# Kernel optimization log

Hardware: AMD Instinct MI355X
Metric: run time of the kernel (lower is better)

Reference implementation:

```python
import jax, jax.numpy as jnp
import numpy as np

B, T, N, F_IN = 32, 64, 128, 16
H, SOUT = 64, 16
D = N * SOUT            # transformer d_model = 2048
NHEADS, DH = 16, 128
DFF, LAYERS = 2048, 2
NCLASSES, OUT = 8, 10
THR = 0.004             # edge threshold on sigmoid(V)/N


def setup_inputs():
    key = jax.random.key(0)
    ks = iter(jax.random.split(key, 40))
    r = lambda *s: jax.random.normal(next(ks), s, jnp.float32) * 0.02
    return {
        'X': jax.random.normal(next(ks), (B, T, N * F_IN), jnp.float32),
        'V_Adap': jax.random.normal(next(ks), (NCLASSES, N, N), jnp.float32),
        'Wl': r(F_IN, H), 'bl': jnp.zeros((H,)),
        'Wr': r(F_IN, H), 'br': jnp.zeros((H,)),
        'att': jax.random.normal(next(ks), (H,), jnp.float32) * 0.1,
        'gat_bias': jnp.zeros((H,)),
        'Wfc': r(H, SOUT), 'bfc': jnp.zeros((SOUT,)),
        'Wq': r(LAYERS, D, D), 'bq': jnp.zeros((LAYERS, D)),
        'Wk': r(LAYERS, D, D), 'bk': jnp.zeros((LAYERS, D)),
        'Wv': r(LAYERS, D, D), 'bv': jnp.zeros((LAYERS, D)),
        'Wo': r(LAYERS, D, D), 'bo': jnp.zeros((LAYERS, D)),
        'ln1_g': jnp.ones((LAYERS, D)), 'ln1_b': jnp.zeros((LAYERS, D)),
        'W1': r(LAYERS, D, DFF), 'b1': jnp.zeros((LAYERS, DFF)),
        'W2': r(LAYERS, DFF, D), 'b2': jnp.zeros((LAYERS, D)),
        'ln2_g': jnp.ones((LAYERS, D)), 'ln2_b': jnp.zeros((LAYERS, D)),
        'Wout': r(D, OUT), 'bout': jnp.zeros((OUT,)),
        'class_idx': 2,
    }


def _ln(x, g, b):
    mu = jnp.mean(x, -1, keepdims=True)
    var = jnp.var(x, -1, keepdims=True)
    return (x - mu) / jnp.sqrt(var + 1e-5) * g + b


def reference(X, V_Adap, Wl, bl, Wr, br, att, gat_bias, Wfc, bfc,
              Wq, bq, Wk, bk, Wv, bv, Wo, bo, ln1_g, ln1_b,
              W1, b1, W2, b2, ln2_g, ln2_b, Wout, bout, class_idx):
    # dynamic adjacency: sigmoid + scale + threshold (data-dependent sparsity as a mask)
    A = jax.nn.sigmoid(V_Adap[class_idx]) / N
    mask = (A > THR) | jnp.eye(N, dtype=bool)   # GATv2Conv default add_self_loops

    def gat_step(x_t):                           # x_t: (B, N, F_IN)
        xl = x_t @ Wl + bl                       # source transform (B, N, H)
        xr = x_t @ Wr + br                       # target transform (B, N, H)
        s = jax.nn.leaky_relu(xl[:, :, None, :] + xr[:, None, :, :], 0.2)  # (B, src, dst, H)
        e = jnp.where(mask[None], jnp.einsum('bijh,h->bij', s, att), -1e9)
        alpha = jax.nn.softmax(e, axis=1)        # softmax over sources per target node
        out = jnp.einsum('bij,bih->bjh', alpha, xl) + gat_bias
        return out @ Wfc + bfc                   # (B, N, SOUT)

    Xr = X.reshape(B, T, N, F_IN).transpose(1, 0, 2, 3)   # (T, B, N, F)
    spatial = jax.lax.map(gat_step, Xr)                   # (T, B, N, SOUT)
    h = spatial.transpose(1, 0, 2, 3).reshape(B, T, D)

    # post-norm TransformerEncoder (torch defaults: relu, d_ff=2048, no dropout at eval)
    for l in range(LAYERS):
        q = (h @ Wq[l] + bq[l]).reshape(B, T, NHEADS, DH).transpose(0, 2, 1, 3)
        k = (h @ Wk[l] + bk[l]).reshape(B, T, NHEADS, DH).transpose(0, 2, 1, 3)
        v = (h @ Wv[l] + bv[l]).reshape(B, T, NHEADS, DH).transpose(0, 2, 1, 3)
        aw = jax.nn.softmax(jnp.einsum('bhqd,bhkd->bhqk', q, k) / np.float32(np.sqrt(DH)), axis=-1)
        ao = jnp.einsum('bhqk,bhkd->bhqd', aw, v).transpose(0, 2, 1, 3).reshape(B, T, D)
        h = _ln(h + ao @ Wo[l] + bo[l], ln1_g[l], ln1_b[l])
        ff = jax.nn.relu(h @ W1[l] + b1[l]) @ W2[l] + b2[l]
        h = _ln(h + ff, ln2_g[l], ln2_b[l])

    return h[:, -1, :] @ Wout + bout             # (B, OUT)
```

## Files before the change

kernel.cpp:

```cpp
#include <hip/hip_runtime.h>
#include <cstdint>
#include <cstddef>


typedef unsigned short u16;
typedef __bf16 bf16x8 __attribute__((ext_vector_type(8)));
typedef float f32x4 __attribute__((ext_vector_type(4)));
typedef unsigned int u32x4 __attribute__((ext_vector_type(4)));
typedef float f32x4v __attribute__((ext_vector_type(4)));
typedef unsigned short u16x4 __attribute__((ext_vector_type(4)));

__device__ __forceinline__ u16 f2b(float f) {
  union { float f; unsigned u; } x; x.f = f;
  unsigned r = x.u + 0x7fffu + ((x.u >> 16) & 1u);
  return (u16)(r >> 16);
}
__device__ __forceinline__ float b2f(u16 s) {
  union { unsigned u; float f; } x; x.u = ((unsigned)s) << 16;
  return x.f;
}
__device__ __forceinline__ float b2f_lo(unsigned q) {
  union { unsigned u; float f; } x; x.u = q << 16;
  return x.f;
}
__device__ __forceinline__ float b2f_hi(unsigned q) {
  union { unsigned u; float f; } x; x.u = q & 0xffff0000u;
  return x.f;
}

__device__ __forceinline__ void gload_lds16(const void* g, void* l) {
  __builtin_amdgcn_global_load_lds(
      (const __attribute__((address_space(1))) unsigned int*)g,
      (__attribute__((address_space(3))) unsigned int*)l, 16, 0, 0);
}

__global__ __launch_bounds__(1024) void gat_kernel(
    const float* __restrict__ X, const float* __restrict__ V_Adap,
    const int* __restrict__ class_idx,
    const float* __restrict__ Wl, const float* __restrict__ bl,
    const float* __restrict__ Wr, const float* __restrict__ br,
    const float* __restrict__ att, const float* __restrict__ gat_bias,
    const float* __restrict__ Wfc, const float* __restrict__ bfc,
    float* __restrict__ h_f32, u16* __restrict__ h_b16)
{
  const int bt = blockIdx.x;
  const int tid = threadIdx.x;

  __shared__ __align__(16) float xlT[64 * 132];
  __shared__ __align__(16) float xrT[64 * 132];
  __shared__ __align__(16) u16   xlTb[64 * 136];
  __shared__ __align__(16) u16   esbT[128 * 136];
  __shared__ __align__(16) u16   aggb[128 * 72];
  __shared__ __align__(16) float WlT[64 * 20];
  __shared__ __align__(16) float WrT[64 * 20];
  __shared__ __align__(16) float WfcT[16 * 66];
  __shared__ float atts[64], bls[64], brs[64], gbias[64], bfcs[16];
  __shared__ float cls[128], crs[128], inv_s[128];
  __shared__ float red[8 * 128];

  {
    const int h = tid >> 4, f = tid & 15;
    WlT[h * 20 + f] = Wl[f * 64 + h];
    WrT[h * 20 + f] = Wr[f * 64 + h];
    WfcT[f * 66 + h] = Wfc[h * 16 + f];
  }
  if (tid < 64) { atts[tid] = att[tid]; bls[tid] = bl[tid]; brs[tid] = br[tid]; gbias[tid] = gat_bias[tid]; }
  if (tid < 16) bfcs[tid] = bfc[tid];
  const int cidx = *class_idx;
  __syncthreads();

  {
    const int n = tid >> 3, hq = tid & 7;
    const float* xp = X + (size_t)bt * 2048 + n * 16;
    float xv[16];
    #pragma unroll
    for (int f4 = 0; f4 < 4; f4++) {
      f32x4v t4 = ((const f32x4v*)xp)[f4];
      xv[f4 * 4 + 0] = t4[0]; xv[f4 * 4 + 1] = t4[1];
      xv[f4 * 4 + 2] = t4[2]; xv[f4 * 4 + 3] = t4[3];
    }
    #pragma unroll
    for (int k = 0; k < 8; k++) {
      const int h = hq + 8 * k;
      float al = bls[h], ar = brs[h];
      #pragma unroll
      for (int f4 = 0; f4 < 4; f4++) {
        f32x4v wl = *(const f32x4v*)&WlT[h * 20 + f4 * 4];
        f32x4v wr = *(const f32x4v*)&WrT[h * 20 + f4 * 4];
        #pragma unroll
        for (int f = 0; f < 4; f++) {
          al = fmaf(xv[f4 * 4 + f], wl[f], al);
          ar = fmaf(xv[f4 * 4 + f], wr[f], ar);
        }
      }
      xlT[h * 132 + n] = al;
      xrT[h * 132 + n] = ar;
      xlTb[h * 136 + n] = f2b(al);
    }
  }
  __syncthreads();

  if (tid < 256) {
    const int n = tid & 127;
    const float* srcT = (tid < 128) ? xlT : xrT;
    float s = 0.f;
    for (int h = 0; h < 64; h++) s = fmaf(atts[h], srcT[h * 132 + n], s);
    if (tid < 128) cls[n] = s; else crs[n] = s;
  }
  __syncthreads();

  {
    const int i0 = (tid >> 5) * 4;
    const int j0 = (tid & 31) * 4;
    float acc[4][4] = {};
    #pragma unroll 2
    for (int h = 0; h < 64; h++) {
      const float ah = atts[h];
      f32x4v xa = *(const f32x4v*)&xlT[h * 132 + i0];
      f32x4v xb = *(const f32x4v*)&xrT[h * 132 + j0];
      #pragma unroll
      for (int a = 0; a < 4; a++)
        #pragma unroll
        for (int b = 0; b < 4; b++)
          acc[a][b] = fmaf(ah, __builtin_fabsf(xa[a] + xb[b]), acc[a][b]);
    }
    const float* Vc = V_Adap + (size_t)cidx * 16384;
    float vm[4][4];
    #pragma unroll
    for (int a = 0; a < 4; a++) {
      f32x4v vc = *(const f32x4v*)&Vc[(size_t)(i0 + a) * 128 + j0];
      #pragma unroll
      for (int b = 0; b < 4; b++) vm[a][b] = vc[b];
    }
    #pragma unroll
    for (int b = 0; b < 4; b++) {
      const int j = j0 + b;
      const float ej = 0.6f * crs[j];
      u16x4 pk;
      #pragma unroll
      for (int a = 0; a < 4; a++) {
        const int i = i0 + a;
        const float e = ej + 0.6f * cls[i] + 0.4f * acc[a][b];
        const bool m = (vm[a][b] > 0.04800922f) || (i == j);
        pk[a] = f2b(m ? e : -1e9f);
      }
      *(u16x4*)&esbT[j * 136 + i0] = pk;
    }
  }
  __syncthreads();

  {
    const int j = tid >> 3, c = tid & 7;
    u16* rp = &esbT[j * 136 + c * 16];
    float ps = 0.f;
    #pragma unroll
    for (int half = 0; half < 2; half++) {
      u32x4 q = *(u32x4*)(rp + half * 8);
      #pragma unroll
      for (int w2 = 0; w2 < 4; w2++) {
        const float p0 = __expf(b2f_lo(q[w2]));
        const float p1 = __expf(b2f_hi(q[w2]));
        ps += p0 + p1;
        q[w2] = (unsigned)f2b(p0) | ((unsigned)f2b(p1) << 16);
      }
      *(u32x4*)(rp + half * 8) = q;
    }
    red[c * 128 + j] = ps;
  }
  __syncthreads();
  if (tid < 128) {
    float s = 0.f;
    #pragma unroll
    for (int c = 0; c < 8; c++) s += red[c * 128 + tid];
    inv_s[tid] = 1.f / s;
  }
  __syncthreads();

  {
    const int w = tid >> 6, lane = tid & 63;
    const int lq = lane >> 4, lr = lane & 15;
    const int jt = w >> 1, ht0 = (w & 1) * 2;
    f32x4 acc2[2] = {};
    #pragma unroll
    for (int ks = 0; ks < 4; ks++) {
      const bf16x8 af = __builtin_bit_cast(bf16x8,
          *(const u32x4*)&esbT[(jt * 16 + lr) * 136 + ks * 32 + lq * 8]);
      #pragma unroll
      for (int t = 0; t < 2; t++) {
        const bf16x8 bfb = __builtin_bit_cast(bf16x8,
            *(const u32x4*)&xlTb[((ht0 + t) * 16 + lr) * 136 + ks * 32 + lq * 8]);
        acc2[t] = __builtin_amdgcn_mfma_f32_16x16x32_bf16(af, bfb, acc2[t], 0, 0, 0);
      }
    }
    #pragma unroll
    for (int t = 0; t < 2; t++) {
      const int h = (ht0 + t) * 16 + lr;
      const float gb = gbias[h];
      #pragma unroll
      for (int r = 0; r < 4; r++) {
        const int j = jt * 16 + lq * 4 + r;
        aggb[j * 72 + h] = f2b(acc2[t][r] * inv_s[j] + gb);
      }
    }
  }
  __syncthreads();

  {
    const int j = tid >> 3, s0 = (tid & 7) * 2;
    float o0 = bfcs[s0], o1 = bfcs[s0 + 1];
    #pragma unroll
    for (int h8 = 0; h8 < 8; h8++) {
      u32x4 q = *(const u32x4*)&aggb[j * 72 + h8 * 8];
      #pragma unroll
      for (int w2 = 0; w2 < 4; w2++) {
        const int h = h8 * 8 + w2 * 2;
        const float a0 = b2f_lo(q[w2]);
        const float a1 = b2f_hi(q[w2]);
        o0 = fmaf(a0, WfcT[s0 * 66 + h], o0);
        o1 = fmaf(a0, WfcT[(s0 + 1) * 66 + h], o1);
        o0 = fmaf(a1, WfcT[s0 * 66 + h + 1], o0);
        o1 = fmaf(a1, WfcT[(s0 + 1) * 66 + h + 1], o1);
      }
    }
    const size_t off = (size_t)bt * 2048 + j * 16 + s0;
    h_f32[off] = o0; h_f32[off + 1] = o1;
    h_b16[off] = f2b(o0); h_b16[off + 1] = f2b(o1);
  }
}

struct TransArgs {
  const float* s0; const float* s1; const float* s2;
  u16* d0; u16* d1; u16* d2;
};

__global__ __launch_bounds__(256) void transpose_cast(TransArgs p)
{
  const float* src = (blockIdx.z == 0) ? p.s0 : (blockIdx.z == 1) ? p.s1 : p.s2;
  u16* dst = (blockIdx.z == 0) ? p.d0 : (blockIdx.z == 1) ? p.d1 : p.d2;
  __shared__ u16 tile[64][66];
  const int k0 = blockIdx.y * 64, n0 = blockIdx.x * 64;
  const int tid = threadIdx.x;
  const int c = tid & 63, rb = tid >> 6;
  #pragma unroll
  for (int r = 0; r < 16; r++) {
    const int k = rb + r * 4;
    tile[k][c] = f2b(src[(size_t)(k0 + k) * 2048 + n0 + c]);
  }
  __syncthreads();
  #pragma unroll
  for (int r = 0; r < 16; r++) {
    const int n = rb + r * 4;
    dst[(size_t)(n0 + n) * 2048 + k0 + c] = tile[c][n];
  }
}

struct GemmArgs {
  const u16* A;
  const u16* Bt0; const u16* Bt1; const u16* Bt2;
  const float* b0; const float* b1; const float* b2;
  void* C0; void* C1; void* C2;
  int N; int K;
};

template <int MODE>
__global__ __launch_bounds__(256) void gemm_bt(GemmArgs g)
{
  const int z = blockIdx.z;
  const u16* Bt = (z == 0) ? g.Bt0 : (z == 1) ? g.Bt1 : g.Bt2;
  const float* bias = (z == 0) ? g.b0 : (z == 1) ? g.b1 : g.b2;
  void* C = (z == 0) ? g.C0 : (z == 1) ? g.C1 : g.C2;
  const int N = g.N, K = g.K;
  const int m0 = blockIdx.y * 128, n0 = blockIdx.x * 128;

  __shared__ __align__(16) u16 As[128 * 32];
  __shared__ __align__(16) u16 Bs[128 * 32];

  const int tid = threadIdx.x;
  const int lane = tid & 63, w = tid >> 6;
  const int srow = w * 16 + (lane >> 2);
  const int scol = (lane & 3) * 8;
  const u16* gA = g.A + (size_t)(m0 + srow) * K + scol;
  const u16* gB = Bt + (size_t)(n0 + srow) * K + scol;
  u16* lA0 = &As[(w * 16) * 32];
  u16* lA1 = &As[(64 + w * 16) * 32];
  u16* lB0 = &Bs[(w * 16) * 32];
  u16* lB1 = &Bs[(64 + w * 16) * 32];

  const int wm = (w >> 1) * 64, wn = (w & 1) * 64;
  const int lq = lane >> 4, lr = lane & 15;

  f32x4 acc[4][4] = {};

  for (int k0 = 0; k0 < K; k0 += 32) {
    gload_lds16(gA + k0, lA0);
    gload_lds16(gA + (size_t)64 * K + k0, lA1);
    gload_lds16(gB + k0, lB0);
    gload_lds16(gB + (size_t)64 * K + k0, lB1);
    __syncthreads();

    bf16x8 af[4], bf[4];
    #pragma unroll
    for (int i = 0; i < 4; i++) {
      af[i] = __builtin_bit_cast(bf16x8, *(const u32x4*)&As[(wm + i * 16 + lr) * 32 + lq * 8]);
      bf[i] = __builtin_bit_cast(bf16x8, *(const u32x4*)&Bs[(wn + i * 16 + lr) * 32 + lq * 8]);
    }
    #pragma unroll
    for (int mi = 0; mi < 4; mi++)
      #pragma unroll
      for (int ni = 0; ni < 4; ni++)
        acc[mi][ni] = __builtin_amdgcn_mfma_f32_16x16x32_bf16(af[mi], bf[ni], acc[mi][ni], 0, 0, 0);
    __syncthreads();
  }

  #pragma unroll
  for (int ni = 0; ni < 4; ni++) {
    const int col = n0 + wn + ni * 16 + lr;
    const float bv = bias[col];
    #pragma unroll
    for (int mi = 0; mi < 4; mi++) {
      #pragma unroll
      for (int r = 0; r < 4; r++) {
        const int row = m0 + wm + mi * 16 + lq * 4 + r;
        float v = acc[mi][ni][r] + bv;
        if (MODE == 0) {
          ((float*)C)[(size_t)row * N + col] = v;
        } else {
          if (MODE == 2) v = fmaxf(v, 0.f);
          ((u16*)C)[(size_t)row * N + col] = f2b(v);
        }
      }
    }
  }
}

template <int MODE>
__global__ __launch_bounds__(256) void gemm_bt64(GemmArgs g)
{
  const u16* Bt = g.Bt0;
  const float* bias = g.b0;
  void* C = g.C0;
  const int N = g.N, K = g.K;
  const int m0 = blockIdx.y * 128, n0 = blockIdx.x * 64;

  __shared__ __align__(16) u16 As[128 * 32];
  __shared__ __align__(16) u16 Bs[64 * 32];

  const int tid = threadIdx.x;
  const int lane = tid & 63, w = tid >> 6;
  const int srow = w * 16 + (lane >> 2);
  const int scol = (lane & 3) * 8;
  const u16* gA = g.A + (size_t)(m0 + srow) * K + scol;
  const u16* gB = Bt + (size_t)(n0 + srow) * K + scol;
  u16* lA0 = &As[(w * 16) * 32];
  u16* lA1 = &As[(64 + w * 16) * 32];
  u16* lB0 = &Bs[(w * 16) * 32];

  const int wm = w * 32;
  const int lq = lane >> 4, lr = lane & 15;

  f32x4 acc[2][4] = {};

  for (int k0 = 0; k0 < K; k0 += 32) {
    gload_lds16(gA + k0, lA0);
    gload_lds16(gA + (size_t)64 * K + k0, lA1);
    gload_lds16(gB + k0, lB0);
    __syncthreads();

    bf16x8 af[2], bf[4];
    #pragma unroll
    for (int i = 0; i < 2; i++)
      af[i] = __builtin_bit_cast(bf16x8, *(const u32x4*)&As[(wm + i * 16 + lr) * 32 + lq * 8]);
    #pragma unroll
    for (int i = 0; i < 4; i++)
      bf[i] = __builtin_bit_cast(bf16x8, *(const u32x4*)&Bs[(i * 16 + lr) * 32 + lq * 8]);
    #pragma unroll
    for (int mi = 0; mi < 2; mi++)
      #pragma unroll
      for (int ni = 0; ni < 4; ni++)
        acc[mi][ni] = __builtin_amdgcn_mfma_f32_16x16x32_bf16(af[mi], bf[ni], acc[mi][ni], 0, 0, 0);
    __syncthreads();
  }

  #pragma unroll
  for (int ni = 0; ni < 4; ni++) {
    const int col = n0 + ni * 16 + lr;
    const float bv = bias[col];
    #pragma unroll
    for (int mi = 0; mi < 2; mi++) {
      #pragma unroll
      for (int r = 0; r < 4; r++) {
        const int row = m0 + wm + mi * 16 + lq * 4 + r;
        float v = acc[mi][ni][r] + bv;
        if (MODE == 0) {
          ((float*)C)[(size_t)row * N + col] = v;
        } else {
          if (MODE == 2) v = fmaxf(v, 0.f);
          ((u16*)C)[(size_t)row * N + col] = f2b(v);
        }
      }
    }
  }
}

__global__ __launch_bounds__(256) void attn_kernel(
    const u16* __restrict__ Qb, const u16* __restrict__ Kb,
    const u16* __restrict__ Vb, u16* __restrict__ AOb)
{
  const int head = blockIdx.x, b = blockIdx.y;
  const int tid = threadIdx.x;
  __shared__ __align__(16) float qs[64 * 129];
  __shared__ __align__(16) float ks[64 * 129];
  __shared__ __align__(16) float vs[64 * 128];
  __shared__ __align__(16) float ss[64 * 65];
  const size_t base = ((size_t)b * 64) * 2048 + (size_t)head * 128;

  for (int idx = tid; idx < 8192; idx += 256) {
    const int t_ = idx >> 7, d = idx & 127;
    const size_t gp = base + (size_t)t_ * 2048 + d;
    qs[t_ * 129 + d] = b2f(Qb[gp]);
    ks[t_ * 129 + d] = b2f(Kb[gp]);
    vs[t_ * 128 + d] = b2f(Vb[gp]);
  }
  __syncthreads();

  {
    const int i0 = (tid >> 4) * 4, j0 = (tid & 15) * 4;
    float acc[4][4] = {};
    for (int d = 0; d < 128; d++) {
      float qv[4], kv[4];
      #pragma unroll
      for (int a = 0; a < 4; a++) qv[a] = qs[(i0 + a) * 129 + d];
      #pragma unroll
      for (int c = 0; c < 4; c++) kv[c] = ks[(j0 + c) * 129 + d];
      #pragma unroll
      for (int a = 0; a < 4; a++)
        #pragma unroll
        for (int c = 0; c < 4; c++)
          acc[a][c] = fmaf(qv[a], kv[c], acc[a][c]);
    }
    const float sc = 0.08838834764831845f;
    #pragma unroll
    for (int a = 0; a < 4; a++)
      #pragma unroll
      for (int c = 0; c < 4; c++)
        ss[(i0 + a) * 65 + j0 + c] = acc[a][c] * sc;
  }
  __syncthreads();

  if (tid < 64) {
    float mx = -3e38f;
    for (int j = 0; j < 64; j++) mx = fmaxf(mx, ss[tid * 65 + j]);
    float s = 0.f;
    for (int j = 0; j < 64; j++) {
      const float p = __expf(ss[tid * 65 + j] - mx);
      ss[tid * 65 + j] = p; s += p;
    }
    const float inv = 1.f / s;
    for (int j = 0; j < 64; j++) ss[tid * 65 + j] *= inv;
  }
  __syncthreads();

  {
    const int i0 = (tid >> 4) * 4, d0 = (tid & 15) * 8;
    float o[4][8] = {};
    for (int j = 0; j < 64; j++) {
      float pv[4];
      #pragma unroll
      for (int a = 0; a < 4; a++) pv[a] = ss[(i0 + a) * 65 + j];
      f32x4v v0 = *(const f32x4v*)&vs[j * 128 + d0];
      f32x4v v1 = *(const f32x4v*)&vs[j * 128 + d0 + 4];
      float vv[8] = {v0[0], v0[1], v0[2], v0[3], v1[0], v1[1], v1[2], v1[3]};
      #pragma unroll
      for (int a = 0; a < 4; a++)
        #pragma unroll
        for (int c = 0; c < 8; c++)
          o[a][c] = fmaf(pv[a], vv[c], o[a][c]);
    }
    #pragma unroll
    for (int a = 0; a < 4; a++)
      #pragma unroll
      for (int c = 0; c < 8; c++)
        AOb[base + (size_t)(i0 + a) * 2048 + d0 + c] = f2b(o[a][c]);
  }
}

__global__ __launch_bounds__(256) void ln_kernel(
    const float* __restrict__ hin, const float* __restrict__ delta,
    const float* __restrict__ gamma, const float* __restrict__ beta,
    float* __restrict__ hout, u16* __restrict__ bout_)
{
  const int token = blockIdx.x, tid = threadIdx.x;
  const size_t off = (size_t)token * 2048;
  __shared__ float red[8];
  float v[8];
  float s = 0.f;
  #pragma unroll
  for (int r = 0; r < 8; r++) {
    const int i = r * 256 + tid;
    v[r] = hin[off + i] + delta[off + i];
    s += v[r];
  }
  #pragma unroll
  for (int o = 32; o > 0; o >>= 1) s += __shfl_down(s, o, 64);
  if ((tid & 63) == 0) red[tid >> 6] = s;
  __syncthreads();
  const float mean = (red[0] + red[1] + red[2] + red[3]) * (1.f / 2048.f);
  float s2 = 0.f;
  #pragma unroll
  for (int r = 0; r < 8; r++) { const float d = v[r] - mean; s2 = fmaf(d, d, s2); }
  #pragma unroll
  for (int o = 32; o > 0; o >>= 1) s2 += __shfl_down(s2, o, 64);
  if ((tid & 63) == 0) red[4 + (tid >> 6)] = s2;
  __syncthreads();
  const float var = (red[4] + red[5] + red[6] + red[7]) * (1.f / 2048.f);
  const float rstd = rsqrtf(var + 1e-5f);
  #pragma unroll
  for (int r = 0; r < 8; r++) {
    const int i = r * 256 + tid;
    const float y = (v[r] - mean) * rstd * gamma[i] + beta[i];
    hout[off + i] = y;
    bout_[off + i] = f2b(y);
  }
}

__global__ __launch_bounds__(256) void final_kernel(
    const float* __restrict__ h, const float* __restrict__ Wout,
    const float* __restrict__ bout, float* __restrict__ out)
{
  const int b = blockIdx.x, tid = threadIdx.x;
  __shared__ float row[2048];
  __shared__ float part[256];
  const float* hr = h + ((size_t)b * 64 + 63) * 2048;
  for (int i = tid; i < 2048; i += 256) row[i] = hr[i];
  __syncthreads();
  const int o = tid & 15, ch = tid >> 4;
  float s = 0.f;
  if (o < 10) {
    const int i0 = ch * 128;
    for (int i = i0; i < i0 + 128; i++) s = fmaf(row[i], Wout[(size_t)i * 10 + o], s);
  }
  part[tid] = s;
  __syncthreads();
  if (tid < 10) {
    float t = bout[tid];
    for (int c2 = 0; c2 < 16; c2++) t += part[c2 * 16 + tid];
    out[(size_t)b * 10 + tid] = t;
  }
}

extern "C" void kernel_launch(void* const* d_in, const int* in_sizes, int n_in,
                              void* d_out, int out_size, void* d_ws, size_t ws_size,
                              hipStream_t stream)
{
  const float* X        = (const float*)d_in[0];
  const float* V_Adap   = (const float*)d_in[1];
  const float* Wl       = (const float*)d_in[2];
  const float* bl       = (const float*)d_in[3];
  const float* Wr       = (const float*)d_in[4];
  const float* br       = (const float*)d_in[5];
  const float* att      = (const float*)d_in[6];
  const float* gat_bias = (const float*)d_in[7];
  const float* Wfc      = (const float*)d_in[8];
  const float* bfc      = (const float*)d_in[9];
  const float* Wq       = (const float*)d_in[10];
  const float* bq       = (const float*)d_in[11];
  const float* Wk       = (const float*)d_in[12];
  const float* bk       = (const float*)d_in[13];
  const float* Wv       = (const float*)d_in[14];
  const float* bv       = (const float*)d_in[15];
  const float* Wo       = (const float*)d_in[16];
  const float* bo       = (const float*)d_in[17];
  const float* ln1_g    = (const float*)d_in[18];
  const float* ln1_b    = (const float*)d_in[19];
  const float* W1       = (const float*)d_in[20];
  const float* b1       = (const float*)d_in[21];
  const float* W2       = (const float*)d_in[22];
  const float* b2       = (const float*)d_in[23];
  const float* ln2_g    = (const float*)d_in[24];
  const float* ln2_b    = (const float*)d_in[25];
  const float* WoutP    = (const float*)d_in[26];
  const float* boutP    = (const float*)d_in[27];
  const int*   class_idx = (const int*)d_in[28];

  char* ws = (char*)d_ws;
  const size_t MB = (size_t)1 << 20;
  float* h_f32 = (float*)(ws);
  u16*   h_b16 = (u16*)(ws + 16 * MB);
  u16*   Qb    = (u16*)(ws + 24 * MB);
  u16*   Kb    = (u16*)(ws + 32 * MB);
  u16*   Vb    = (u16*)(ws + 40 * MB);
  u16*   AOb   = (u16*)(ws + 48 * MB);
  float* tmp   = (float*)(ws + 56 * MB);
  u16*   ff1b  = (u16*)(ws + 72 * MB);
  u16*   Wt0   = (u16*)(ws + 80 * MB);
  u16*   Wt1   = (u16*)(ws + 88 * MB);
  u16*   Wt2   = (u16*)(ws + 96 * MB);

  gat_kernel<<<2048, 1024, 0, stream>>>(X, V_Adap, class_idx, Wl, bl, Wr, br,
                                        att, gat_bias, Wfc, bfc, h_f32, h_b16);

  const size_t DD = 2048ull * 2048ull;
  for (int l = 0; l < 2; l++) {
    const size_t wofs = (size_t)l * DD;
    const size_t bofs = (size_t)l * 2048;

    transpose_cast<<<dim3(32, 32, 3), 256, 0, stream>>>(
        TransArgs{Wq + wofs, Wk + wofs, Wv + wofs, Wt0, Wt1, Wt2});
    gemm_bt<1><<<dim3(16, 16, 3), 256, 0, stream>>>(
        GemmArgs{h_b16, Wt0, Wt1, Wt2, bq + bofs, bk + bofs, bv + bofs,
                 Qb, Kb, Vb, 2048, 2048});

    attn_kernel<<<dim3(16, 32), 256, 0, stream>>>(Qb, Kb, Vb, AOb);

    transpose_cast<<<dim3(32, 32, 3), 256, 0, stream>>>(
        TransArgs{Wo + wofs, W1 + wofs, W2 + wofs, Wt0, Wt1, Wt2});

    gemm_bt64<0><<<dim3(32, 16), 256, 0, stream>>>(
        GemmArgs{AOb, Wt0, nullptr, nullptr, bo + bofs, nullptr, nullptr,
                 tmp, nullptr, nullptr, 2048, 2048});
    ln_kernel<<<2048, 256, 0, stream>>>(h_f32, tmp, ln1_g + bofs, ln1_b + bofs,
                                        h_f32, h_b16);

    gemm_bt64<2><<<dim3(32, 16), 256, 0, stream>>>(
        GemmArgs{h_b16, Wt1, nullptr, nullptr, b1 + bofs, nullptr, nullptr,
                 ff1b, nullptr, nullptr, 2048, 2048});

    gemm_bt64<0><<<dim3(32, 16), 256, 0, stream>>>(
        GemmArgs{ff1b, Wt2, nullptr, nullptr, b2 + bofs, nullptr, nullptr,
                 tmp, nullptr, nullptr, 2048, 2048});
    ln_kernel<<<2048, 256, 0, stream>>>(h_f32, tmp, ln2_g + bofs, ln2_b + bofs,
                                        h_f32, h_b16);
  }

  final_kernel<<<32, 256, 0, stream>>>(h_f32, WoutP, boutP, (float*)d_out);
}
```

Baseline: 966.5 us.

## Use MFMA attention, split-K GEMMs with fused bias/LN combine, bf16 GAT scores

Attention scores and P·V now use bf16 MFMA instructions in place of scalar fp32 loops, and the softmax normalisation is folded into the output scaling. The 128x64-tile GEMMs are replaced by 128x128-tile split-K GEMMs that write two fp32 partials; the bias, the partial sums and the ReLU are applied in the LayerNorm kernel or in a new combine kernel. The GAT edge-score loop now stores att-scaled bf16 values in a swizzled layout and uses packed two-wide adds, which cuts shared-memory footprint and load count but lowers the precision of the scores. The split-K path adds an extra fp32 partial round trip through memory, and the second partial buffer reuses the Q buffer region.

```diff
diff --git a/kernel.cpp b/kernel.cpp
--- a/kernel.cpp
+++ b/kernel.cpp
@@ -6,6 +6,7 @@
 typedef unsigned short u16;
 typedef __bf16 bf16x8 __attribute__((ext_vector_type(8)));
 typedef float f32x4 __attribute__((ext_vector_type(4)));
+typedef float f32x2 __attribute__((ext_vector_type(2)));
 typedef unsigned int u32x4 __attribute__((ext_vector_type(4)));
 typedef float f32x4v __attribute__((ext_vector_type(4)));
 typedef unsigned short u16x4 __attribute__((ext_vector_type(4)));
@@ -46,15 +47,16 @@
   const int bt = blockIdx.x;
   const int tid = threadIdx.x;
 
-  __shared__ __align__(16) float xlT[64 * 132];
-  __shared__ __align__(16) float xrT[64 * 132];
+  __shared__ __align__(16) u16   xl2b[128 * 64];
+  __shared__ __align__(16) u16   xr2b[128 * 64];
   __shared__ __align__(16) u16   xlTb[64 * 136];
   __shared__ __align__(16) u16   esbT[128 * 136];
   __shared__ __align__(16) u16   aggb[128 * 72];
   __shared__ __align__(16) float WlT[64 * 20];
   __shared__ __align__(16) float WrT[64 * 20];
   __shared__ __align__(16) float WfcT[16 * 66];
-  __shared__ float atts[64], bls[64], brs[64], gbias[64], bfcs[16];
+  __shared__ __align__(16) float sgns[64];
+  __shared__ float aab[64], bls[64], brs[64], gbias[64], bfcs[16];
   __shared__ float cls[128], crs[128], inv_s[128];
   __shared__ float red[8 * 128];
 
@@ -64,13 +66,19 @@
     WrT[h * 20 + f] = Wr[f * 64 + h];
     WfcT[f * 66 + h] = Wfc[h * 16 + f];
   }
-  if (tid < 64) { atts[tid] = att[tid]; bls[tid] = bl[tid]; brs[tid] = br[tid]; gbias[tid] = gat_bias[tid]; }
+  if (tid < 64) {
+    const float a = att[tid];
+    aab[tid] = __builtin_fabsf(a);
+    sgns[tid] = (a >= 0.f) ? 1.f : -1.f;
+    bls[tid] = bl[tid]; brs[tid] = br[tid]; gbias[tid] = gat_bias[tid];
+  }
   if (tid < 16) bfcs[tid] = bfc[tid];
   const int cidx = *class_idx;
   __syncthreads();
 
   {
     const int n = tid >> 3, hq = tid & 7;
+    const int sw = (n >> 2) & 7;
     const float* xp = X + (size_t)bt * 2048 + n * 16;
     float xv[16];
     #pragma unroll
@@ -93,36 +101,74 @@
           ar = fmaf(xv[f4 * 4 + f], wr[f], ar);
         }
       }
-      xlT[h * 132 + n] = al;
-      xrT[h * 132 + n] = ar;
       xlTb[h * 136 + n] = f2b(al);
+      const float sc = aab[h];
+      const int pos = n * 64 + ((k ^ sw) << 3) + hq;
+      xl2b[pos] = f2b(al * sc);
+      xr2b[pos] = f2b(ar * sc);
     }
   }
   __syncthreads();
 
   if (tid < 256) {
     const int n = tid & 127;
-    const float* srcT = (tid < 128) ? xlT : xrT;
+    const u16* src = (tid < 128) ? xl2b : xr2b;
+    const int sw = (n >> 2) & 7;
     float s = 0.f;
-    for (int h = 0; h < 64; h++) s = fmaf(atts[h], srcT[h * 132 + n], s);
+    #pragma unroll
+    for (int sl = 0; sl < 8; sl++) {
+      const int c = sl ^ sw;
+      u32x4 q = *(const u32x4*)&src[n * 64 + sl * 8];
+      f32x4v g0 = *(const f32x4v*)&sgns[c * 8];
+      f32x4v g1 = *(const f32x4v*)&sgns[c * 8 + 4];
+      s += g0[0] * b2f_lo(q[0]) + g0[1] * b2f_hi(q[0])
+         + g0[2] * b2f_lo(q[1]) + g0[3] * b2f_hi(q[1]);
+      s += g1[0] * b2f_lo(q[2]) + g1[1] * b2f_hi(q[2])
+         + g1[2] * b2f_lo(q[3]) + g1[3] * b2f_hi(q[3]);
+    }
     if (tid < 128) cls[n] = s; else crs[n] = s;
   }
   __syncthreads();
 
   {
-    const int i0 = (tid >> 5) * 4;
-    const int j0 = (tid & 31) * 4;
+    const int i0 = (tid >> 5) * 4, j0 = (tid & 31) * 4;
+    const int swi = (i0 >> 2) & 7, swj = (j0 >> 2) & 7;
     float acc[4][4] = {};
     #pragma unroll 2
-    for (int h = 0; h < 64; h++) {
-      const float ah = atts[h];
-      f32x4v xa = *(const f32x4v*)&xlT[h * 132 + i0];
-      f32x4v xb = *(const f32x4v*)&xrT[h * 132 + j0];
+    for (int hc = 0; hc < 8; hc++) {
+      u32x4 ua[4], ub[4];
       #pragma unroll
       for (int a = 0; a < 4; a++)
+        ua[a] = *(const u32x4*)&xl2b[(i0 + a) * 64 + ((hc ^ swi) << 3)];
+      #pragma unroll
+      for (int b = 0; b < 4; b++)
+        ub[b] = *(const u32x4*)&xr2b[(j0 + b) * 64 + ((hc ^ swj) << 3)];
+      f32x4v g0 = *(const f32x4v*)&sgns[hc * 8];
+      f32x4v g1 = *(const f32x4v*)&sgns[hc * 8 + 4];
+      #pragma unroll
+      for (int ep = 0; ep < 4; ep++) {
+        const float s0 = (ep < 2) ? g0[(ep & 1) * 2]     : g1[(ep & 1) * 2];
+        const float s1 = (ep < 2) ? g0[(ep & 1) * 2 + 1] : g1[(ep & 1) * 2 + 1];
+        f32x2 xap[4], xbp[4];
         #pragma unroll
-        for (int b = 0; b < 4; b++)
-          acc[a][b] = fmaf(ah, __builtin_fabsf(xa[a] + xb[b]), acc[a][b]);
+        for (int a = 0; a < 4; a++) {
+          const unsigned q = ua[a][ep];
+          xap[a] = (f32x2){b2f_lo(q), b2f_hi(q)};
+        }
+        #pragma unroll
+        for (int b = 0; b < 4; b++) {
+          const unsigned q = ub[b][ep];
+          xbp[b] = (f32x2){b2f_lo(q), b2f_hi(q)};
+        }
+        #pragma unroll
+        for (int a = 0; a < 4; a++)
+          #pragma unroll
+          for (int b = 0; b < 4; b++) {
+            const f32x2 z = xap[a] + xbp[b];
+            acc[a][b] = fmaf(s0, __builtin_fabsf(z[0]), acc[a][b]);
+            acc[a][b] = fmaf(s1, __builtin_fabsf(z[1]), acc[a][b]);
+          }
+      }
     }
     const float* Vc = V_Adap + (size_t)cidx * 16384;
     float vm[4][4];
@@ -262,7 +308,6 @@
   int N; int K;
 };
 
-template <int MODE>
 __global__ __launch_bounds__(256) void gemm_bt(GemmArgs g)
 {
   const int z = blockIdx.z;
@@ -322,59 +367,59 @@
       for (int r = 0; r < 4; r++) {
         const int row = m0 + wm + mi * 16 + lq * 4 + r;
         float v = acc[mi][ni][r] + bv;
-        if (MODE == 0) {
-          ((float*)C)[(size_t)row * N + col] = v;
-        } else {
-          if (MODE == 2) v = fmaxf(v, 0.f);
-          ((u16*)C)[(size_t)row * N + col] = f2b(v);
-        }
-      }
-    }
-  }
-}
-
-template <int MODE>
-__global__ __launch_bounds__(256) void gemm_bt64(GemmArgs g)
-{
-  const u16* Bt = g.Bt0;
-  const float* bias = g.b0;
-  void* C = g.C0;
-  const int N = g.N, K = g.K;
-  const int m0 = blockIdx.y * 128, n0 = blockIdx.x * 64;
+        ((u16*)C)[(size_t)row * N + col] = f2b(v);
+      }
+    }
+  }
+}
+
+struct GemmKArgs {
+  const u16* A; const u16* Bt;
+  float* C0; float* C1;
+  int N; int K;
+};
+
+__global__ __launch_bounds__(256) void gemm_splitk(GemmKArgs g)
+{
+  const int z = blockIdx.z;
+  float* C = z ? g.C1 : g.C0;
+  const int N = g.N, K = g.K, kbase = z * (K >> 1);
+  const int m0 = blockIdx.y * 128, n0 = blockIdx.x * 128;
 
   __shared__ __align__(16) u16 As[128 * 32];
-  __shared__ __align__(16) u16 Bs[64 * 32];
+  __shared__ __align__(16) u16 Bs[128 * 32];
 
   const int tid = threadIdx.x;
   const int lane = tid & 63, w = tid >> 6;
   const int srow = w * 16 + (lane >> 2);
   const int scol = (lane & 3) * 8;
-  const u16* gA = g.A + (size_t)(m0 + srow) * K + scol;
-  const u16* gB = Bt + (size_t)(n0 + srow) * K + scol;
+  const u16* gA = g.A + (size_t)(m0 + srow) * K + kbase + scol;
+  const u16* gB = g.Bt + (size_t)(n0 + srow) * K + kbase + scol;
   u16* lA0 = &As[(w * 16) * 32];
   u16* lA1 = &As[(64 + w * 16) * 32];
   u16* lB0 = &Bs[(w * 16) * 32];
-
-  const int wm = w * 32;
+  u16* lB1 = &Bs[(64 + w * 16) * 32];
+
+  const int wm = (w >> 1) * 64, wn = (w & 1) * 64;
   const int lq = lane >> 4, lr = lane & 15;
 
-  f32x4 acc[2][4] = {};
-
-  for (int k0 = 0; k0 < K; k0 += 32) {
+  f32x4 acc[4][4] = {};
+
+  for (int k0 = 0; k0 < (K >> 1); k0 += 32) {
     gload_lds16(gA + k0, lA0);
     gload_lds16(gA + (size_t)64 * K + k0, lA1);
     gload_lds16(gB + k0, lB0);
+    gload_lds16(gB + (size_t)64 * K + k0, lB1);
     __syncthreads();
 
-    bf16x8 af[2], bf[4];
-    #pragma unroll
-    for (int i = 0; i < 2; i++)
+    bf16x8 af[4], bf[4];
+    #pragma unroll
+    for (int i = 0; i < 4; i++) {
       af[i] = __builtin_bit_cast(bf16x8, *(const u32x4*)&As[(wm + i * 16 + lr) * 32 + lq * 8]);
-    #pragma unroll
-    for (int i = 0; i < 4; i++)
-      bf[i] = __builtin_bit_cast(bf16x8, *(const u32x4*)&Bs[(i * 16 + lr) * 32 + lq * 8]);
-    #pragma unroll
-    for (int mi = 0; mi < 2; mi++)
+      bf[i] = __builtin_bit_cast(bf16x8, *(const u32x4*)&Bs[(wn + i * 16 + lr) * 32 + lq * 8]);
+    }
+    #pragma unroll
+    for (int mi = 0; mi < 4; mi++)
       #pragma unroll
       for (int ni = 0; ni < 4; ni++)
         acc[mi][ni] = __builtin_amdgcn_mfma_f32_16x16x32_bf16(af[mi], bf[ni], acc[mi][ni], 0, 0, 0);
@@ -383,20 +428,13 @@
 
   #pragma unroll
   for (int ni = 0; ni < 4; ni++) {
-    const int col = n0 + ni * 16 + lr;
-    const float bv = bias[col];
-    #pragma unroll
-    for (int mi = 0; mi < 2; mi++) {
+    const int col = n0 + wn + ni * 16 + lr;
+    #pragma unroll
+    for (int mi = 0; mi < 4; mi++) {
       #pragma unroll
       for (int r = 0; r < 4; r++) {
         const int row = m0 + wm + mi * 16 + lq * 4 + r;
-        float v = acc[mi][ni][r] + bv;
-        if (MODE == 0) {
-          ((float*)C)[(size_t)row * N + col] = v;
-        } else {
-          if (MODE == 2) v = fmaxf(v, 0.f);
-          ((u16*)C)[(size_t)row * N + col] = f2b(v);
-        }
+        C[(size_t)row * N + col] = acc[mi][ni][r];
       }
     }
   }
@@ -408,84 +446,109 @@
 {
   const int head = blockIdx.x, b = blockIdx.y;
   const int tid = threadIdx.x;
-  __shared__ __align__(16) float qs[64 * 129];
-  __shared__ __align__(16) float ks[64 * 129];
-  __shared__ __align__(16) float vs[64 * 128];
-  __shared__ __align__(16) float ss[64 * 65];
+  const int lane = tid & 63, w = tid >> 6;
+  const int lq = lane >> 4, lr = lane & 15;
+
+  __shared__ __align__(16) char smA[2 * 64 * 136 * 2];
+  __shared__ __align__(16) u16 vsT[128 * 72];
+  __shared__ float sred[256], sinv[64];
+
+  u16* qsb = (u16*)smA;
+  u16* ksb = qsb + 64 * 136;
   const size_t base = ((size_t)b * 64) * 2048 + (size_t)head * 128;
 
-  for (int idx = tid; idx < 8192; idx += 256) {
-    const int t_ = idx >> 7, d = idx & 127;
-    const size_t gp = base + (size_t)t_ * 2048 + d;
-    qs[t_ * 129 + d] = b2f(Qb[gp]);
-    ks[t_ * 129 + d] = b2f(Kb[gp]);
-    vs[t_ * 128 + d] = b2f(Vb[gp]);
-  }
-  __syncthreads();
-
-  {
-    const int i0 = (tid >> 4) * 4, j0 = (tid & 15) * 4;
-    float acc[4][4] = {};
-    for (int d = 0; d < 128; d++) {
-      float qv[4], kv[4];
-      #pragma unroll
-      for (int a = 0; a < 4; a++) qv[a] = qs[(i0 + a) * 129 + d];
-      #pragma unroll
-      for (int c = 0; c < 4; c++) kv[c] = ks[(j0 + c) * 129 + d];
-      #pragma unroll
-      for (int a = 0; a < 4; a++)
-        #pragma unroll
-        for (int c = 0; c < 4; c++)
-          acc[a][c] = fmaf(qv[a], kv[c], acc[a][c]);
-    }
+  for (int idx = tid; idx < 1024; idx += 256) {
+    const int t = idx >> 4, c = idx & 15;
+    const size_t gp = base + (size_t)t * 2048 + c * 8;
+    u32x4 q4 = *(const u32x4*)(Qb + gp);
+    u32x4 k4 = *(const u32x4*)(Kb + gp);
+    u32x4 v4 = *(const u32x4*)(Vb + gp);
+    *(u32x4*)&qsb[t * 136 + c * 8] = q4;
+    *(u32x4*)&ksb[t * 136 + c * 8] = k4;
+    const int tcc = t >> 3, t7 = t & 7;
+    #pragma unroll
+    for (int e = 0; e < 8; e++) {
+      const int d = c * 8 + e;
+      const unsigned q = v4[e >> 1];
+      const u16 val = (e & 1) ? (u16)(q >> 16) : (u16)(q & 0xffffu);
+      vsT[d * 72 + ((tcc ^ ((d >> 3) & 7)) << 3) + t7] = val;
+    }
+  }
+  __syncthreads();
+
+  f32x4 sacc[4] = {};
+  #pragma unroll
+  for (int ks = 0; ks < 4; ks++) {
+    const bf16x8 af = __builtin_bit_cast(bf16x8,
+        *(const u32x4*)&qsb[(w * 16 + lr) * 136 + ks * 32 + lq * 8]);
+    #pragma unroll
+    for (int jt = 0; jt < 4; jt++) {
+      const bf16x8 bfb = __builtin_bit_cast(bf16x8,
+          *(const u32x4*)&ksb[(jt * 16 + lr) * 136 + ks * 32 + lq * 8]);
+      sacc[jt] = __builtin_amdgcn_mfma_f32_16x16x32_bf16(af, bfb, sacc[jt], 0, 0, 0);
+    }
+  }
+  __syncthreads();
+
+  float* ssf = (float*)smA;
+  u16* psb = (u16*)smA + 64 * 136;
+  {
     const float sc = 0.08838834764831845f;
     #pragma unroll
-    for (int a = 0; a < 4; a++)
-      #pragma unroll
-      for (int c = 0; c < 4; c++)
-        ss[(i0 + a) * 65 + j0 + c] = acc[a][c] * sc;
-  }
-  __syncthreads();
-
-  if (tid < 64) {
-    float mx = -3e38f;
-    for (int j = 0; j < 64; j++) mx = fmaxf(mx, ss[tid * 65 + j]);
-    float s = 0.f;
-    for (int j = 0; j < 64; j++) {
-      const float p = __expf(ss[tid * 65 + j] - mx);
-      ss[tid * 65 + j] = p; s += p;
-    }
-    const float inv = 1.f / s;
-    for (int j = 0; j < 64; j++) ss[tid * 65 + j] *= inv;
-  }
-  __syncthreads();
-
-  {
-    const int i0 = (tid >> 4) * 4, d0 = (tid & 15) * 8;
-    float o[4][8] = {};
-    for (int j = 0; j < 64; j++) {
-      float pv[4];
-      #pragma unroll
-      for (int a = 0; a < 4; a++) pv[a] = ss[(i0 + a) * 65 + j];
-      f32x4v v0 = *(const f32x4v*)&vs[j * 128 + d0];
-      f32x4v v1 = *(const f32x4v*)&vs[j * 128 + d0 + 4];
-      float vv[8] = {v0[0], v0[1], v0[2], v0[3], v1[0], v1[1], v1[2], v1[3]};
-      #pragma unroll
-      for (int a = 0; a < 4; a++)
-        #pragma unroll
-        for (int c = 0; c < 8; c++)
-          o[a][c] = fmaf(pv[a], vv[c], o[a][c]);
-    }
-    #pragma unroll
-    for (int a = 0; a < 4; a++)
-      #pragma unroll
-      for (int c = 0; c < 8; c++)
-        AOb[base + (size_t)(i0 + a) * 2048 + d0 + c] = f2b(o[a][c]);
-  }
-}
-
-__global__ __launch_bounds__(256) void ln_kernel(
-    const float* __restrict__ hin, const float* __restrict__ delta,
+    for (int jt = 0; jt < 4; jt++)
+      #pragma unroll
+      for (int r = 0; r < 4; r++)
+        ssf[(w * 16 + lq * 4 + r) * 68 + jt * 16 + lr] = sacc[jt][r] * sc;
+  }
+  __syncthreads();
+
+  {
+    const int i = tid >> 2, c = tid & 3;
+    float ps = 0.f;
+    #pragma unroll
+    for (int cc = 0; cc < 4; cc++) {
+      f32x4v s4 = *(const f32x4v*)&ssf[i * 68 + c * 16 + cc * 4];
+      float p0 = __expf(s4[0]), p1 = __expf(s4[1]);
+      float p2 = __expf(s4[2]), p3 = __expf(s4[3]);
+      ps += p0 + p1 + p2 + p3;
+      u16x4 pk = {f2b(p0), f2b(p1), f2b(p2), f2b(p3)};
+      *(u16x4*)&psb[i * 136 + c * 16 + cc * 4] = pk;
+    }
+    sred[tid] = ps;
+  }
+  __syncthreads();
+  if (tid < 64)
+    sinv[tid] = 1.f / (sred[tid * 4] + sred[tid * 4 + 1] + sred[tid * 4 + 2] + sred[tid * 4 + 3]);
+  __syncthreads();
+
+  {
+    f32x4 oacc[8] = {};
+    #pragma unroll
+    for (int ks = 0; ks < 2; ks++) {
+      const bf16x8 af = __builtin_bit_cast(bf16x8,
+          *(const u32x4*)&psb[(w * 16 + lr) * 136 + ks * 32 + lq * 8]);
+      #pragma unroll
+      for (int dt = 0; dt < 8; dt++) {
+        const int d = dt * 16 + lr;
+        const bf16x8 bfb = __builtin_bit_cast(bf16x8,
+            *(const u32x4*)&vsT[d * 72 + (((ks * 4 + lq) ^ ((d >> 3) & 7)) << 3)]);
+        oacc[dt] = __builtin_amdgcn_mfma_f32_16x16x32_bf16(af, bfb, oacc[dt], 0, 0, 0);
+      }
+    }
+    #pragma unroll
+    for (int r = 0; r < 4; r++) {
+      const int i = w * 16 + lq * 4 + r;
+      const float inv = sinv[i];
+      #pragma unroll
+      for (int dt = 0; dt < 8; dt++)
+        AOb[base + (size_t)i * 2048 + dt * 16 + lr] = f2b(oacc[dt][r] * inv);
+    }
+  }
+}
+
+__global__ __launch_bounds__(256) void ln_kernel2(
+    const float* __restrict__ hin, const float* __restrict__ d0,
+    const float* __restrict__ d1, const float* __restrict__ bias,
     const float* __restrict__ gamma, const float* __restrict__ beta,
     float* __restrict__ hout, u16* __restrict__ bout_)
 {
@@ -497,7 +560,7 @@
   #pragma unroll
   for (int r = 0; r < 8; r++) {
     const int i = r * 256 + tid;
-    v[r] = hin[off + i] + delta[off + i];
+    v[r] = hin[off + i] + d0[off + i] + d1[off + i] + bias[i];
     s += v[r];
   }
   #pragma unroll
@@ -521,6 +584,21 @@
     hout[off + i] = y;
     bout_[off + i] = f2b(y);
   }
+}
+
+__global__ __launch_bounds__(256) void combine_relu(
+    const float* __restrict__ d0, const float* __restrict__ d1,
+    const float* __restrict__ bias, u16* __restrict__ out)
+{
+  const size_t idx = ((size_t)blockIdx.x * 256 + threadIdx.x) * 4;
+  const int col = (int)(idx & 2047);
+  f32x4v a = *(const f32x4v*)(d0 + idx);
+  f32x4v c = *(const f32x4v*)(d1 + idx);
+  f32x4v bv = *(const f32x4v*)(bias + col);
+  u16x4 o;
+  #pragma unroll
+  for (int e = 0; e < 4; e++) o[e] = f2b(fmaxf(a[e] + c[e] + bv[e], 0.f));
+  *(u16x4*)(out + idx) = o;
 }
 
 __global__ __launch_bounds__(256) void final_kernel(
@@ -590,7 +668,8 @@
   u16*   Kb    = (u16*)(ws + 32 * MB);
   u16*   Vb    = (u16*)(ws + 40 * MB);
   u16*   AOb   = (u16*)(ws + 48 * MB);
-  float* tmp   = (float*)(ws + 56 * MB);
+  float* tmp0  = (float*)(ws + 56 * MB);
+  float* tmp1  = (float*)(ws + 24 * MB);
   u16*   ff1b  = (u16*)(ws + 72 * MB);
   u16*   Wt0   = (u16*)(ws + 80 * MB);
   u16*   Wt1   = (u16*)(ws + 88 * MB);
@@ -606,7 +685,7 @@
 
     transpose_cast<<<dim3(32, 32, 3), 256, 0, stream>>>(
         TransArgs{Wq + wofs, Wk + wofs, Wv + wofs, Wt0, Wt1, Wt2});
-    gemm_bt<1><<<dim3(16, 16, 3), 256, 0, stream>>>(
+    gemm_bt<<<dim3(16, 16, 3), 256, 0, stream>>>(
         GemmArgs{h_b16, Wt0, Wt1, Wt2, bq + bofs, bk + bofs, bv + bofs,
                  Qb, Kb, Vb, 2048, 2048});
 
@@ -615,21 +694,21 @@
     transpose_cast<<<dim3(32, 32, 3), 256, 0, stream>>>(
         TransArgs{Wo + wofs, W1 + wofs, W2 + wofs, Wt0, Wt1, Wt2});
 
-    gemm_bt64<0><<<dim3(32, 16), 256, 0, stream>>>(
-        GemmArgs{AOb, Wt0, nullptr, nullptr, bo + bofs, nullptr, nullptr,
-                 tmp, nullptr, nullptr, 2048, 2048});
-    ln_kernel<<<2048, 256, 0, stream>>>(h_f32, tmp, ln1_g + bofs, ln1_b + bofs,
-                                        h_f32, h_b16);
-
-    gemm_bt64<2><<<dim3(32, 16), 256, 0, stream>>>(
-        GemmArgs{h_b16, Wt1, nullptr, nullptr, b1 + bofs, nullptr, nullptr,
-                 ff1b, nullptr, nullptr, 2048, 2048});
-
-    gemm_bt64<0><<<dim3(32, 16), 256, 0, stream>>>(
-        GemmArgs{ff1b, Wt2, nullptr, nullptr, b2 + bofs, nullptr, nullptr,
-                 tmp, nullptr, nullptr, 2048, 2048});
-    ln_kernel<<<2048, 256, 0, stream>>>(h_f32, tmp, ln2_g + bofs, ln2_b + bofs,
-                                        h_f32, h_b16);
+    gemm_splitk<<<dim3(16, 16, 2), 256, 0, stream>>>(
+        GemmKArgs{AOb, Wt0, tmp0, tmp1, 2048, 2048});
+    ln_kernel2<<<2048, 256, 0, stream>>>(h_f32, tmp0, tmp1, bo + bofs,
+                                         ln1_g + bofs, ln1_b + bofs,
+                                         h_f32, h_b16);
+
+    gemm_splitk<<<dim3(16, 16, 2), 256, 0, stream>>>(
+        GemmKArgs{h_b16, Wt1, tmp0, tmp1, 2048, 2048});
+    combine_relu<<<4096, 256, 0, stream>>>(tmp0, tmp1, b1 + bofs, ff1b);
+
+    gemm_splitk<<<dim3(16, 16, 2), 256, 0, stream>>>(
+        GemmKArgs{ff1b, Wt2, tmp0, tmp1, 2048, 2048});
+    ln_kernel2<<<2048, 256, 0, stream>>>(h_f32, tmp0, tmp1, b2 + bofs,
+                                         ln2_g + bofs, ln2_b + bofs,
+                                         h_f32, h_b16);
   }
 
   final_kernel<<<32, 256, 0, stream>>>(h_f32, WoutP, boutP, (float*)d_out);
```

Measured after the change: 1.019 ms. +5.5%, slower.
